# Performance work log

Measured on AMD Instinct MI355X. Metric: run time of the kernel, lower is better.

## Reference

```python
import jax, jax.numpy as jnp
import numpy as np

B, S, HID, NH, KCLIP = 2, 1500, 1024, 16, 64
HD = HID // NH  # 64


def setup_inputs() -> dict:
    key = jax.random.key(0)
    ks = jax.random.split(key, 16)
    std = 0.02
    inp = {
        "query": jax.random.normal(ks[0], (B, S, HID), jnp.float32),
        "key": jax.random.normal(ks[1], (B, S, HID), jnp.float32),
        "value": jax.random.normal(ks[2], (B, S, HID), jnp.float32),
        # per-head projection weights, stacked over heads: [NH, HID, HD]
        "Wq": jax.random.normal(ks[3], (NH, HID, HD), jnp.float32) * std,
        "bq": jax.random.normal(ks[4], (NH, HD), jnp.float32) * std,
        "Wk": jax.random.normal(ks[5], (NH, HID, HD), jnp.float32) * std,
        "bk": jax.random.normal(ks[6], (NH, HD), jnp.float32) * std,
        "Wv": jax.random.normal(ks[7], (NH, HID, HD), jnp.float32) * std,
        "bv": jax.random.normal(ks[8], (NH, HD), jnp.float32) * std,
        # Shaw relative-position embedding tables: [2k+1, HD]
        "pe_k": jax.random.normal(ks[9], (2 * KCLIP + 1, HD), jnp.float32) * std,
        "pe_v": jax.random.normal(ks[10], (2 * KCLIP + 1, HD), jnp.float32) * std,
        # output projection (torch Linear stored as x @ W + b here)
        "W_fc": jax.random.normal(ks[11], (HID, HID), jnp.float32) * std,
        "b_fc": jax.random.normal(ks[12], (HID,), jnp.float32) * std,
    }
    return inp


def _rel_bias(pe, length, k_clip):
    idx = jnp.arange(length)
    dist = jnp.clip(idx[None, :] - idx[:, None], -k_clip, k_clip) + k_clip
    return pe[dist]  # [S, S, HD]


def reference(query, key, value, Wq, bq, Wk, bk, Wv, bv, pe_k, pe_v, W_fc, b_fc):
    head_dim = Wq.shape[-1]
    seq = query.shape[1]
    k_clip = (pe_k.shape[0] - 1) // 2

    kb = _rel_bias(pe_k, seq, k_clip)  # [S, S, HD]
    vb = _rel_bias(pe_v, seq, k_clip)  # [S, S, HD]

    # batched per-head projections: [B, NH, S, HD]
    Q = jnp.einsum('bsh,nhd->bnsd', query, Wq) + bq[None, :, None, :]
    K = jnp.einsum('bsh,nhd->bnsd', key, Wk) + bk[None, :, None, :]
    V = jnp.einsum('bsh,nhd->bnsd', value, Wv) + bv[None, :, None, :]

    # content term + Shaw relative-key bias term
    scores = jnp.einsum('bnqd,bnkd->bnqk', Q, K) \
           + jnp.einsum('bnqd,qkd->bnqk', Q, kb)
    scores = scores / jnp.sqrt(jnp.asarray(head_dim, scores.dtype))

    w = jax.nn.softmax(scores, axis=-1)  # [B, NH, S, S]

    out = jnp.einsum('bnqk,bnkd->bnqd', w, V) \
        + jnp.einsum('bnqk,qkd->bnqd', w, vb)

    # concat heads (head order matches ModuleList concatenation)
    hidden = out.transpose(0, 2, 1, 3).reshape(query.shape[0], seq, -1)
    return hidden @ W_fc + b_fc
```

## Files before the change

### kernel.cpp

```cpp
#include <hip/hip_runtime.h>
#include <math.h>

#define B_     2
#define S_     1500
#define HID_   1024
#define NH_    16
#define HD_    64
#define M_     (B_*S_)
#define SP_    1536

typedef short bf16x8 __attribute__((ext_vector_type(8)));
typedef short bf16x4 __attribute__((ext_vector_type(4)));
typedef float f32x4  __attribute__((ext_vector_type(4)));

__device__ __forceinline__ float b2f(short s) {
    unsigned u = ((unsigned)(unsigned short)s) << 16;
    return __uint_as_float(u);
}
__device__ __forceinline__ short f2b(float f) {
    unsigned u = __float_as_uint(f);
    unsigned r = (u + 0x7FFFu + ((u >> 16) & 1u)) >> 16;
    return (short)r;
}
__device__ __forceinline__ void gload16(const short* src, short* lds) {
    __builtin_amdgcn_global_load_lds(
        (const __attribute__((address_space(1))) void*)src,
        (__attribute__((address_space(3))) void*)lds, 16, 0, 0);
}

__global__ __launch_bounds__(256) void cvt_act3(
    const float* __restrict__ q, const float* __restrict__ k,
    const float* __restrict__ v, short* __restrict__ oq,
    short* __restrict__ ok, short* __restrict__ ov)
{
    const float* src = blockIdx.y == 0 ? q : blockIdx.y == 1 ? k : v;
    short* dst       = blockIdx.y == 0 ? oq : blockIdx.y == 1 ? ok : ov;
    int i = blockIdx.x * 256 + threadIdx.x;
    const float4* p = (const float4*)(src + (size_t)i * 8);
    float4 a = p[0], b = p[1];
    bf16x8 o;
    o[0]=f2b(a.x); o[1]=f2b(a.y); o[2]=f2b(a.z); o[3]=f2b(a.w);
    o[4]=f2b(b.x); o[5]=f2b(b.y); o[6]=f2b(b.z); o[7]=f2b(b.w);
    *(bf16x8*)(dst + (size_t)i * 8) = o;
}

__global__ __launch_bounds__(256) void prep_w(
    const float* __restrict__ Wq, const float* __restrict__ Wk,
    const float* __restrict__ Wv, const float* __restrict__ Wfc,
    const float* __restrict__ pe_k, const float* __restrict__ pe_v,
    short* __restrict__ Wqt, short* __restrict__ Wkt, short* __restrict__ Wvt,
    short* __restrict__ Wfh, short* __restrict__ Wfl,
    short* __restrict__ pe_kb, short* __restrict__ pe_vt)
{
    int z = blockIdx.x, tid = threadIdx.x;
    if (z == 1024) {
        for (int s = tid; s < 144 * 64; s += 256) {
            int j = s >> 6, d = s & 63;
            pe_kb[s] = (j < 129) ? f2b(pe_k[j * 64 + d]) : (short)0;
        }
        for (int s = tid; s < 64 * 160; s += 256) {
            int d = s / 160, j = s - d * 160;
            pe_vt[s] = (j < 129) ? f2b(pe_v[j * 64 + d]) : (short)0;
        }
        return;
    }
    __shared__ float T[64][65];
    const float* src; short* dhi; short* dlo = nullptr;
    int C, c0, r0; float scale = 1.f;
    if (z < 768) {
        int widx = z >> 8, rem = z & 255;
        int h = rem >> 4, rt = rem & 15;
        src = (widx == 0 ? Wq : widx == 1 ? Wk : Wv) + (size_t)h * 1024 * 64;
        dhi = (widx == 0 ? Wqt : widx == 1 ? Wkt : Wvt) + (size_t)h * 64 * 1024;
        scale = (widx == 0) ? 0.125f : 1.0f;
        C = 64; c0 = 0; r0 = rt * 64;
    } else {
        int idx = z - 768;
        src = Wfc; dhi = Wfh; dlo = Wfl;
        C = 1024; c0 = (idx >> 4) * 64; r0 = (idx & 15) * 64;
    }
#pragma unroll
    for (int i = 0; i < 4; ++i) {
        int slot = tid + i * 256;
        int r = slot >> 4, cg = (slot & 15) * 4;
        float4 v = *(const float4*)(src + (size_t)(r0 + r) * C + c0 + cg);
        T[r][cg+0] = v.x*scale; T[r][cg+1] = v.y*scale;
        T[r][cg+2] = v.z*scale; T[r][cg+3] = v.w*scale;
    }
    __syncthreads();
#pragma unroll
    for (int i = 0; i < 16; ++i) {
        int slot = tid + i * 256;
        int c = slot >> 6, r = slot & 63;
        float v = T[r][c];
        short hi = f2b(v);
        size_t o = (size_t)(c0 + c) * 1024 + r0 + r;
        dhi[o] = hi;
        if (dlo) dlo[o] = f2b(v - b2f(hi));
    }
}

__device__ __forceinline__ void gemm_core(
    const short* __restrict__ Ahi, const short* __restrict__ Alo,
    const short* __restrict__ Bhi, const short* __restrict__ Blo,
    int kIters, int m0, int n0, short* As, short* Bs, f32x4 (&acc)[4][4])
{
    const int tid = threadIdx.x, w = tid >> 6, lane = tid & 63;
    const int l15 = lane & 15, lr4 = lane >> 4;
    const int wr = w >> 1, wc = w & 1;

    for (int it = 0; it < kIters; ++it) {
        int kt = it * 64;
        int seg = kt >> 10, kk0 = kt & 1023;
        const short* Aseg = (seg == 1) ? Alo : Ahi;
        const short* Bseg = (seg == 2) ? Blo : Bhi;
        __syncthreads();
#pragma unroll
        for (int c = 0; c < 4; ++c) {
            int slot = (w * 4 + c) * 64 + lane;
            int r = slot >> 3, cb = slot & 7;
            int sm = m0 + r; sm = sm < M_ ? sm : M_ - 1;
            gload16(Aseg + (size_t)sm * 1024 + kk0 + ((cb ^ (r & 7)) * 8),
                    As + (size_t)(w * 4 + c) * 512);
            gload16(Bseg + (size_t)(n0 + r) * 1024 + kk0 + ((cb ^ (r & 7)) * 8),
                    Bs + (size_t)(w * 4 + c) * 512);
        }
        __syncthreads();
#pragma unroll
        for (int kh = 0; kh < 2; ++kh) {
            bf16x8 aF[4], bF[4];
#pragma unroll
            for (int mi = 0; mi < 4; ++mi) {
                int r = wr * 64 + mi * 16 + l15;
                aF[mi] = *(const bf16x8*)(As + r * 64 + (((kh*4+lr4) ^ (r & 7)) * 8));
            }
#pragma unroll
            for (int ni = 0; ni < 4; ++ni) {
                int r = wc * 64 + ni * 16 + l15;
                bF[ni] = *(const bf16x8*)(Bs + r * 64 + (((kh*4+lr4) ^ (r & 7)) * 8));
            }
#pragma unroll
            for (int mi = 0; mi < 4; ++mi)
#pragma unroll
                for (int ni = 0; ni < 4; ++ni)
                    acc[mi][ni] = __builtin_amdgcn_mfma_f32_16x16x32_bf16(
                        aF[mi], bF[ni], acc[mi][ni], 0, 0, 0);
        }
    }
}

__global__ __launch_bounds__(256) void gemm_qkv(
    const short* __restrict__ qb, const short* __restrict__ kb,
    const short* __restrict__ vb, const short* __restrict__ Wqt,
    const short* __restrict__ Wkt, const short* __restrict__ Wvt,
    const float* __restrict__ bq, const float* __restrict__ bk,
    const float* __restrict__ bv,
    short* __restrict__ Qp, short* __restrict__ Kp, short* __restrict__ Vp)
{
    __shared__ short As[128 * 64];
    __shared__ short Bs[128 * 64];
    const int z = blockIdx.z;
    const short* A  = z == 0 ? qb : z == 1 ? kb : vb;
    const short* Bw = z == 0 ? Wqt : z == 1 ? Wkt : Wvt;
    const float* bias = z == 0 ? bq : z == 1 ? bk : bv;
    const float bscale = z == 0 ? 0.125f : 1.0f;
    short* out = z == 0 ? Qp : z == 1 ? Kp : Vp;
    const int m0 = blockIdx.x * 128, n0 = blockIdx.y * 128;

    f32x4 zf = {0.f,0.f,0.f,0.f};
    f32x4 acc[4][4];
#pragma unroll
    for (int i = 0; i < 4; ++i)
#pragma unroll
        for (int j = 0; j < 4; ++j) acc[i][j] = zf;

    gemm_core(A, A, Bw, Bw, 16, m0, n0, As, Bs, acc);

    const int tid = threadIdx.x, w = tid >> 6, lane = tid & 63;
    const int l15 = lane & 15, lr4 = lane >> 4;
    const int wr = w >> 1, wc = w & 1;
#pragma unroll
    for (int mi = 0; mi < 4; ++mi)
#pragma unroll
        for (int rr = 0; rr < 4; ++rr) {
            int m = m0 + wr * 64 + mi * 16 + lr4 * 4 + rr;
            if (m >= M_) continue;
            int b = m / S_, s = m - b * S_;
#pragma unroll
            for (int ni = 0; ni < 4; ++ni) {
                int n = n0 + wc * 64 + ni * 16 + l15;
                float v = acc[mi][ni][rr] + bias[n] * bscale;
                int h = n >> 6, d = n & 63;
                out[(((size_t)(b * NH_ + h)) * S_ + s) * HD_ + d] = f2b(v);
            }
        }
}

__global__ __launch_bounds__(256) void gemm_fc(
    const short* __restrict__ Ahi, const short* __restrict__ Alo,
    const short* __restrict__ Bhi, const short* __restrict__ Blo,
    const float* __restrict__ bias, float* __restrict__ out)
{
    __shared__ short As[128 * 64];
    __shared__ short Bs[128 * 64];
    const int m0 = blockIdx.x * 128, n0 = blockIdx.y * 128;
    f32x4 zf = {0.f,0.f,0.f,0.f};
    f32x4 acc[4][4];
#pragma unroll
    for (int i = 0; i < 4; ++i)
#pragma unroll
        for (int j = 0; j < 4; ++j) acc[i][j] = zf;

    gemm_core(Ahi, Alo, Bhi, Blo, 48, m0, n0, As, Bs, acc);

    const int tid = threadIdx.x, w = tid >> 6, lane = tid & 63;
    const int l15 = lane & 15, lr4 = lane >> 4;
    const int wr = w >> 1, wc = w & 1;
#pragma unroll
    for (int mi = 0; mi < 4; ++mi)
#pragma unroll
        for (int rr = 0; rr < 4; ++rr) {
            int m = m0 + wr * 64 + mi * 16 + lr4 * 4 + rr;
            if (m >= M_) continue;
#pragma unroll
            for (int ni = 0; ni < 4; ++ni) {
                int n = n0 + wc * 64 + ni * 16 + l15;
                out[(size_t)m * 1024 + n] = acc[mi][ni][rr] + bias[n];
            }
        }
}

__global__ __launch_bounds__(256) void vtrans(
    const short* __restrict__ Vp, short* __restrict__ Vtg)
{
    __shared__ short T[64][72];
    const int bh = blockIdx.y, s0 = blockIdx.x * 64, tid = threadIdx.x;
    const size_t kv = (size_t)bh * S_ * 64;
#pragma unroll
    for (int i = 0; i < 2; ++i) {
        int slot = tid + i * 256;
        int r = slot >> 3, cb = slot & 7;
        int ss = s0 + r; ss = ss < S_ ? ss : S_ - 1;
        bf16x8 v = *(const bf16x8*)(Vp + kv + (size_t)ss * 64 + cb * 8);
        *(bf16x8*)(&T[r][cb * 8]) = v;
    }
    __syncthreads();
#pragma unroll
    for (int i = 0; i < 2; ++i) {
        int slot = tid + i * 256;
        int d = slot >> 3, cg = slot & 7;
        bf16x8 v;
#pragma unroll
        for (int j = 0; j < 8; ++j) v[j] = T[cg * 8 + j][d];
        *(bf16x8*)(Vtg + ((size_t)bh * 64 + d) * SP_ + s0 + cg * 8) = v;
    }
}

__global__ __launch_bounds__(256) void attn_mfma(
    const short* __restrict__ Qb, const short* __restrict__ Kb,
    const short* __restrict__ Vtg, const short* __restrict__ pe_kb,
    const short* __restrict__ pe_vt,
    short* __restrict__ hid_hi, short* __restrict__ hid_lo)
{
    __shared__ short Kc[64 * 64];
    __shared__ short Vt[64 * 64];
    __shared__ short qpe[64 * 144];
    __shared__ short wsm[64 * 160];
    __shared__ short Pw[4][16 * 64];

    const int tid = threadIdx.x, w = tid >> 6, lane = tid & 63;
    const int l15 = lane & 15, lr4 = lane >> 4;
    const int bh = blockIdx.y, q0 = blockIdx.x * 64;
    const int qw = q0 + w * 16;
    const int myq = qw + l15;
    const int myrow = w * 16 + l15;
    const size_t kv  = (size_t)bh * S_ * HD_;
    const size_t vtb = (size_t)bh * 64 * SP_;
    const int swz = (l15 & 7) << 1;

    {
        short ini = f2b(-1e30f);
        bf16x8 iv;
#pragma unroll
        for (int i = 0; i < 8; ++i) iv[i] = ini;
        for (int s = tid; s < 64 * 160 / 8; s += 256)
            *(bf16x8*)(wsm + (size_t)s * 8) = iv;
    }
#pragma unroll
    for (int c = 0; c < 2; ++c) {
        int slot = (w * 2 + c) * 64 + lane;
        int r = slot >> 3, cb = slot & 7;
        int sq = q0 + r; sq = sq < S_ ? sq : S_ - 1;
        gload16(Qb + kv + (size_t)sq * 64 + ((cb ^ (r & 7)) * 8),
                Kc + (size_t)(w * 2 + c) * 512);
    }
    __syncthreads();

    bf16x8 qA[2];
    {
        int r = myrow;
        qA[0] = *(const bf16x8*)(Kc + r * 64 + ((lr4 ^ (r & 7)) * 8));
        qA[1] = *(const bf16x8*)(Kc + r * 64 + (((4 + lr4) ^ (r & 7)) * 8));
    }

    f32x4 zf = {0.f,0.f,0.f,0.f};
#pragma unroll
    for (int jt = 0; jt < 9; ++jt) {
        f32x4 a = zf;
#pragma unroll
        for (int kh = 0; kh < 2; ++kh) {
            bf16x8 pf = *(const bf16x8*)(pe_kb + (size_t)(jt * 16 + l15) * 64 + kh * 32 + lr4 * 8);
            a = __builtin_amdgcn_mfma_f32_16x16x32_bf16(pf, qA[kh], a, 0, 0, 0);
        }
        bf16x4 pk;
#pragma unroll
        for (int rr = 0; rr < 4; ++rr) pk[rr] = f2b(a[rr]);
        *(bf16x4*)(qpe + (size_t)myrow * 144 + jt * 16 + lr4 * 4) = pk;
    }
    __syncthreads();

    const float qpe0   = b2f(qpe[myrow * 144 + 0]);
    const float qpe128 = b2f(qpe[myrow * 144 + 128]);

    float m = -1e30f, s0s = 0.f, s1s = 0.f;
    f32x4 o[4];
#pragma unroll
    for (int t = 0; t < 4; ++t) o[t] = zf;

    for (int c = 0; c < 24; ++c) {
        const int kc = c * 64;
        __syncthreads();
#pragma unroll
        for (int cc = 0; cc < 2; ++cc) {
            int slot = (w * 2 + cc) * 64 + lane;
            int r = slot >> 3, cb = slot & 7;
            int sk = kc + r; sk = sk < S_ ? sk : S_ - 1;
            gload16(Kb + kv + (size_t)sk * 64 + ((cb ^ (r & 7)) * 8),
                    Kc + (size_t)(w * 2 + cc) * 512);
            gload16(Vtg + vtb + (size_t)r * SP_ + kc + ((cb ^ (r & 7)) * 8),
                    Vt + (size_t)(w * 2 + cc) * 512);
        }
        __syncthreads();

        f32x4 sa[4];
#pragma unroll
        for (int t = 0; t < 4; ++t) {
            sa[t] = zf;
#pragma unroll
            for (int kh = 0; kh < 2; ++kh) {
                int r = t * 16 + l15;
                bf16x8 kB = *(const bf16x8*)(Kc + r * 64 + (((kh*4+lr4) ^ (r & 7)) * 8));
                sa[t] = __builtin_amdgcn_mfma_f32_16x16x32_bf16(kB, qA[kh], sa[t], 0, 0, 0);
            }
        }

        const bool all_lo = (kc + 63 - qw) <= -64;
        const bool all_hi = (kc - (qw + 15)) >= 64;
        const bool mixed  = !(all_lo || all_hi);
        const float ubias = all_lo ? qpe0 : qpe128;

        float lg[4][4];
        float rm = -1e30f;
#pragma unroll
        for (int t = 0; t < 4; ++t)
#pragma unroll
            for (int rr = 0; rr < 4; ++rr) {
                int k = kc + t * 16 + lr4 * 4 + rr;
                int rel = k - myq;
                float v;
                if (mixed) {
                    int jc = rel < -64 ? 0 : (rel > 64 ? 128 : rel + 64);
                    v = sa[t][rr] + b2f(qpe[myrow * 144 + jc]);
                } else {
                    v = sa[t][rr] + ubias;
                }
                if (k >= S_) v = -1e30f;
                lg[t][rr] = v;
                rm = fmaxf(rm, v);
                if (mixed && rel > -64 && rel < 64)
                    wsm[myrow * 160 + rel + 64] = f2b(v);
            }
        rm = fmaxf(rm, __shfl_xor(rm, 16));
        rm = fmaxf(rm, __shfl_xor(rm, 32));

        if (__any(rm > m)) {
            float nm = fmaxf(m, rm);
            float fac = __expf(m - nm);
            m = nm; s0s *= fac; s1s *= fac;
            float fo[4];
#pragma unroll
            for (int rr = 0; rr < 4; ++rr) fo[rr] = __shfl(fac, lr4 * 4 + rr);
#pragma unroll
            for (int t = 0; t < 4; ++t)
#pragma unroll
                for (int rr = 0; rr < 4; ++rr) o[t][rr] *= fo[rr];
        }

        float ls0 = 0.f, ls1 = 0.f;
#pragma unroll
        for (int t = 0; t < 4; ++t) {
            bf16x4 pk;
#pragma unroll
            for (int rr = 0; rr < 4; ++rr) {
                float p = __expf(lg[t][rr] - m);
                pk[rr] = f2b(p);
                if (mixed) {
                    int rel = (kc + t * 16 + lr4 * 4 + rr) - myq;
                    if (rel <= -64) ls0 += p; else if (rel >= 64) ls1 += p;
                } else if (all_lo) ls0 += p; else ls1 += p;
            }
            *(bf16x4*)(Pw[w] + l15 * 64 + (((t * 4 + lr4) ^ swz) << 2)) = pk;
        }
        ls0 += __shfl_xor(ls0, 16); ls0 += __shfl_xor(ls0, 32);
        ls1 += __shfl_xor(ls1, 16); ls1 += __shfl_xor(ls1, 32);
        s0s += ls0; s1s += ls1;

#pragma unroll
        for (int win = 0; win < 2; ++win) {
            bf16x8 pA = *(const bf16x8*)(Pw[w] + l15 * 64 + (((win * 8 + lr4 * 2) ^ swz) << 2));
#pragma unroll
            for (int td = 0; td < 4; ++td) {
                int r = td * 16 + l15;
                bf16x8 vB = *(const bf16x8*)(Vt + r * 64 + (((win*4+lr4) ^ (r & 7)) * 8));
                o[td] = __builtin_amdgcn_mfma_f32_16x16x32_bf16(pA, vB, o[td], 0, 0, 0);
            }
        }
    }

    short* rowp = wsm + (size_t)myrow * 160;
    float midsum = 0.f;
#pragma unroll
    for (int cc = 0; cc < 5; ++cc) {
        int off = (cc * 4 + lr4) * 8;
        bf16x8 mv = *(const bf16x8*)(rowp + off);
        bf16x8 ev;
#pragma unroll
        for (int jj = 0; jj < 8; ++jj) {
            float e = __expf(b2f(mv[jj]) - m);
            ev[jj] = f2b(e);
            midsum += e;
        }
        *(bf16x8*)(rowp + off) = ev;
    }
    midsum += __shfl_xor(midsum, 16); midsum += __shfl_xor(midsum, 32);
    const float linv = 1.f / (s0s + s1s + midsum);
    if (lr4 == 0) { rowp[0] = f2b(s0s); rowp[128] = f2b(s1s); }

#pragma unroll
    for (int jh = 0; jh < 5; ++jh) {
        bf16x8 aW = *(const bf16x8*)(wsm + (size_t)myrow * 160 + jh * 32 + lr4 * 8);
#pragma unroll
        for (int td = 0; td < 4; ++td) {
            bf16x8 bW = *(const bf16x8*)(pe_vt + (size_t)(td * 16 + l15) * 160 + jh * 32 + lr4 * 8);
            o[td] = __builtin_amdgcn_mfma_f32_16x16x32_bf16(aW, bW, o[td], 0, 0, 0);
        }
    }

    {
        float fo[4];
#pragma unroll
        for (int rr = 0; rr < 4; ++rr) fo[rr] = __shfl(linv, lr4 * 4 + rr);
#pragma unroll
        for (int td = 0; td < 4; ++td)
#pragma unroll
            for (int rr = 0; rr < 4; ++rr) o[td][rr] *= fo[rr];
    }

#pragma unroll
    for (int td = 0; td < 4; ++td)
#pragma unroll
        for (int rr = 0; rr < 4; ++rr) {
            int qrow = lr4 * 4 + rr;
            int d = td * 16 + l15;
            int inner = (((d >> 2) ^ ((qrow & 7) << 1)) << 2) + (d & 3);
            float v = o[td][rr];
            short hi = f2b(v);
            Pw[w][qrow * 64 + inner] = hi;
            wsm[(w * 16 + qrow) * 160 + inner] = f2b(v - b2f(hi));
        }
    {
        int b = bh >> 4, h = bh & 15;
        int qrow = lane >> 2;
        int q = q0 + w * 16 + qrow;
#pragma unroll
        for (int i = 0; i < 2; ++i) {
            int cb = (lane & 3) * 2 + i;
            int qws = (cb * 2) ^ ((qrow & 7) << 1);
            bf16x8 hv = *(const bf16x8*)(Pw[w] + qrow * 64 + qws * 4);
            bf16x8 lv = *(const bf16x8*)(wsm + (w * 16 + qrow) * 160 + qws * 4);
            if (q < S_) {
                size_t oo = ((size_t)(b * S_ + q)) * 1024 + h * 64 + cb * 8;
                *(bf16x8*)(hid_hi + oo) = hv;
                *(bf16x8*)(hid_lo + oo) = lv;
            }
        }
    }
}

extern "C" void kernel_launch(void* const* d_in, const int* in_sizes, int n_in,
                              void* d_out, int out_size, void* d_ws, size_t ws_size,
                              hipStream_t stream)
{
    const float* query = (const float*)d_in[0];
    const float* key   = (const float*)d_in[1];
    const float* value = (const float*)d_in[2];
    const float* Wq    = (const float*)d_in[3];
    const float* bq    = (const float*)d_in[4];
    const float* Wk    = (const float*)d_in[5];
    const float* bk    = (const float*)d_in[6];
    const float* Wv    = (const float*)d_in[7];
    const float* bv    = (const float*)d_in[8];
    const float* pe_k  = (const float*)d_in[9];
    const float* pe_v  = (const float*)d_in[10];
    const float* W_fc  = (const float*)d_in[11];
    const float* b_fc  = (const float*)d_in[12];

    char* W = (char*)d_ws;
    short* qb   = (short*)(W + 0);
    short* kb   = (short*)(W + 6291456);
    short* vb   = (short*)(W + 12582912);
    short* Vtg  = vb;
    short* Wqt  = (short*)(W + 18874368);
    short* Wkt  = (short*)(W + 20971520);
    short* Wvt  = (short*)(W + 23068672);
    short* Wfh  = (short*)(W + 25165824);
    short* Wfl  = (short*)(W + 27262976);
    short* Qp   = (short*)(W + 29360128);
    short* Kp   = (short*)(W + 35651584);
    short* Vp   = (short*)(W + 41943040);
    short* pekb = (short*)(W + 48234496);
    short* pevt = (short*)(W + 48252928);
    short* hidh = qb;
    short* hidl = kb;

    cvt_act3<<<dim3(1500, 3), 256, 0, stream>>>(query, key, value, qb, kb, vb);
    prep_w<<<1025, 256, 0, stream>>>(Wq, Wk, Wv, W_fc, pe_k, pe_v,
                                     Wqt, Wkt, Wvt, Wfh, Wfl, pekb, pevt);
    gemm_qkv<<<dim3(24, 8, 3), 256, 0, stream>>>(qb, kb, vb, Wqt, Wkt, Wvt,
                                                 bq, bk, bv, Qp, Kp, Vp);
    vtrans<<<dim3(24, 32), 256, 0, stream>>>(Vp, Vtg);
    attn_mfma<<<dim3(24, 32), 256, 0, stream>>>(Qp, Kp, Vtg, pekb, pevt, hidh, hidl);
    gemm_fc<<<dim3(24, 8), 256, 0, stream>>>(hidh, hidl, Wfh, Wfl, b_fc, (float*)d_out);
}
```

Baseline: 284.3 us.

## Double-buffer K/V tiles in attention, use exp2 softmax with lazy rescale

The attention kernel now double-buffers the K and V LDS tiles, prefetching the next chunk with async global-to-LDS loads while the current one is computed, and relies on explicit waitcnt plus barriers instead of two __syncthreads per iteration. Q is prescaled by log2(e) so the softmax uses exp2f, and the running-max rescale is skipped unless the max grows by more than 8 (in log2 units). The grid is remapped to a 1D launch with a block swizzle intended to group heads across XCDs, and s_setprio is raised around the MFMA sections. The extra LDS buffers lower occupancy, and the deferred rescale lets intermediate exponentials grow larger, which carries some bf16 precision risk.

```diff
diff --git a/kernel.cpp b/kernel.cpp
--- a/kernel.cpp
+++ b/kernel.cpp
@@ -8,6 +8,7 @@
 #define HD_    64
 #define M_     (B_*S_)
 #define SP_    1536
+#define LOG2E  1.4426950408889634f
 
 typedef short bf16x8 __attribute__((ext_vector_type(8)));
 typedef short bf16x4 __attribute__((ext_vector_type(4)));
@@ -26,6 +27,11 @@
     __builtin_amdgcn_global_load_lds(
         (const __attribute__((address_space(1))) void*)src,
         (__attribute__((address_space(3))) void*)lds, 16, 0, 0);
+}
+__device__ __forceinline__ void bar() {
+    asm volatile("" ::: "memory");
+    __builtin_amdgcn_s_barrier();
+    asm volatile("" ::: "memory");
 }
 
 __global__ __launch_bounds__(256) void cvt_act3(
@@ -72,7 +78,7 @@
         int h = rem >> 4, rt = rem & 15;
         src = (widx == 0 ? Wq : widx == 1 ? Wk : Wv) + (size_t)h * 1024 * 64;
         dhi = (widx == 0 ? Wqt : widx == 1 ? Wkt : Wvt) + (size_t)h * 64 * 1024;
-        scale = (widx == 0) ? 0.125f : 1.0f;
+        scale = (widx == 0) ? 0.125f * LOG2E : 1.0f;
         C = 64; c0 = 0; r0 = rt * 64;
     } else {
         int idx = z - 768;
@@ -163,7 +169,7 @@
     const short* A  = z == 0 ? qb : z == 1 ? kb : vb;
     const short* Bw = z == 0 ? Wqt : z == 1 ? Wkt : Wvt;
     const float* bias = z == 0 ? bq : z == 1 ? bk : bv;
-    const float bscale = z == 0 ? 0.125f : 1.0f;
+    const float bscale = z == 0 ? 0.125f * LOG2E : 1.0f;
     short* out = z == 0 ? Qp : z == 1 ? Kp : Vp;
     const int m0 = blockIdx.x * 128, n0 = blockIdx.y * 128;
 
@@ -262,15 +268,17 @@
     const short* __restrict__ pe_vt,
     short* __restrict__ hid_hi, short* __restrict__ hid_lo)
 {
-    __shared__ short Kc[64 * 64];
-    __shared__ short Vt[64 * 64];
+    __shared__ short Kc[2][4096];
+    __shared__ short Vt[2][4096];
     __shared__ short qpe[64 * 144];
     __shared__ short wsm[64 * 160];
     __shared__ short Pw[4][16 * 64];
 
     const int tid = threadIdx.x, w = tid >> 6, lane = tid & 63;
     const int l15 = lane & 15, lr4 = lane >> 4;
-    const int bh = blockIdx.y, q0 = blockIdx.x * 64;
+    const int lg = (blockIdx.x & 7) * 96 + (blockIdx.x >> 3);
+    const int bh = lg / 24, bx = lg - bh * 24;
+    const int q0 = bx * 64;
     const int qw = q0 + w * 16;
     const int myq = qw + l15;
     const int myrow = w * 16 + l15;
@@ -283,24 +291,37 @@
         bf16x8 iv;
 #pragma unroll
         for (int i = 0; i < 8; ++i) iv[i] = ini;
-        for (int s = tid; s < 64 * 160 / 8; s += 256)
-            *(bf16x8*)(wsm + (size_t)s * 8) = iv;
-    }
-#pragma unroll
-    for (int c = 0; c < 2; ++c) {
-        int slot = (w * 2 + c) * 64 + lane;
+        short* base = wsm + w * 16 * 160;
+#pragma unroll
+        for (int i = 0; i < 5; ++i)
+            *(bf16x8*)(base + (size_t)(i * 64 + lane) * 8) = iv;
+    }
+#pragma unroll
+    for (int cc = 0; cc < 2; ++cc) {
+        int slot = (w * 2 + cc) * 64 + lane;
         int r = slot >> 3, cb = slot & 7;
         int sq = q0 + r; sq = sq < S_ ? sq : S_ - 1;
         gload16(Qb + kv + (size_t)sq * 64 + ((cb ^ (r & 7)) * 8),
-                Kc + (size_t)(w * 2 + c) * 512);
-    }
-    __syncthreads();
+                &Kc[1][(w * 2 + cc) * 512]);
+    }
+#pragma unroll
+    for (int cc = 0; cc < 2; ++cc) {
+        int slot = (w * 2 + cc) * 64 + lane;
+        int r = slot >> 3, cb = slot & 7;
+        gload16(Kb + kv + (size_t)r * 64 + ((cb ^ (r & 7)) * 8),
+                &Kc[0][(w * 2 + cc) * 512]);
+        gload16(Vtg + vtb + (size_t)r * SP_ + ((cb ^ (r & 7)) * 8),
+                &Vt[0][(w * 2 + cc) * 512]);
+    }
+    asm volatile("s_waitcnt vmcnt(4)" ::: "memory");
+    __builtin_amdgcn_s_barrier();
+    asm volatile("" ::: "memory");
 
     bf16x8 qA[2];
     {
         int r = myrow;
-        qA[0] = *(const bf16x8*)(Kc + r * 64 + ((lr4 ^ (r & 7)) * 8));
-        qA[1] = *(const bf16x8*)(Kc + r * 64 + (((4 + lr4) ^ (r & 7)) * 8));
+        qA[0] = *(const bf16x8*)(&Kc[1][r * 64 + ((lr4 ^ (r & 7)) * 8)]);
+        qA[1] = *(const bf16x8*)(&Kc[1][r * 64 + (((4 + lr4) ^ (r & 7)) * 8)]);
     }
 
     f32x4 zf = {0.f,0.f,0.f,0.f};
@@ -317,10 +338,9 @@
         for (int rr = 0; rr < 4; ++rr) pk[rr] = f2b(a[rr]);
         *(bf16x4*)(qpe + (size_t)myrow * 144 + jt * 16 + lr4 * 4) = pk;
     }
-    __syncthreads();
-
     const float qpe0   = b2f(qpe[myrow * 144 + 0]);
     const float qpe128 = b2f(qpe[myrow * 144 + 128]);
+    bar();
 
     float m = -1e30f, s0s = 0.f, s1s = 0.f;
     f32x4 o[4];
@@ -329,19 +349,30 @@
 
     for (int c = 0; c < 24; ++c) {
         const int kc = c * 64;
-        __syncthreads();
-#pragma unroll
-        for (int cc = 0; cc < 2; ++cc) {
-            int slot = (w * 2 + cc) * 64 + lane;
-            int r = slot >> 3, cb = slot & 7;
-            int sk = kc + r; sk = sk < S_ ? sk : S_ - 1;
-            gload16(Kb + kv + (size_t)sk * 64 + ((cb ^ (r & 7)) * 8),
-                    Kc + (size_t)(w * 2 + cc) * 512);
-            gload16(Vtg + vtb + (size_t)r * SP_ + kc + ((cb ^ (r & 7)) * 8),
-                    Vt + (size_t)(w * 2 + cc) * 512);
-        }
-        __syncthreads();
-
+        const int p = c & 1;
+        if (c < 23) {
+            const int kcn = kc + 64;
+            short* KD = Kc[1 - p]; short* VD = Vt[1 - p];
+#pragma unroll
+            for (int cc = 0; cc < 2; ++cc) {
+                int slot = (w * 2 + cc) * 64 + lane;
+                int r = slot >> 3, cb = slot & 7;
+                int sk = kcn + r; sk = sk < S_ ? sk : S_ - 1;
+                gload16(Kb + kv + (size_t)sk * 64 + ((cb ^ (r & 7)) * 8),
+                        KD + (w * 2 + cc) * 512);
+                gload16(Vtg + vtb + (size_t)r * SP_ + kcn + ((cb ^ (r & 7)) * 8),
+                        VD + (w * 2 + cc) * 512);
+            }
+            asm volatile("s_waitcnt vmcnt(4)" ::: "memory");
+        } else {
+            asm volatile("s_waitcnt vmcnt(0)" ::: "memory");
+        }
+        __builtin_amdgcn_s_barrier();
+        asm volatile("" ::: "memory");
+
+        const short* KP = Kc[p]; const short* VP = Vt[p];
+
+        __builtin_amdgcn_s_setprio(1);
         f32x4 sa[4];
 #pragma unroll
         for (int t = 0; t < 4; ++t) {
@@ -349,17 +380,18 @@
 #pragma unroll
             for (int kh = 0; kh < 2; ++kh) {
                 int r = t * 16 + l15;
-                bf16x8 kB = *(const bf16x8*)(Kc + r * 64 + (((kh*4+lr4) ^ (r & 7)) * 8));
+                bf16x8 kB = *(const bf16x8*)(KP + r * 64 + (((kh*4+lr4) ^ (r & 7)) * 8));
                 sa[t] = __builtin_amdgcn_mfma_f32_16x16x32_bf16(kB, qA[kh], sa[t], 0, 0, 0);
             }
         }
+        __builtin_amdgcn_s_setprio(0);
 
         const bool all_lo = (kc + 63 - qw) <= -64;
         const bool all_hi = (kc - (qw + 15)) >= 64;
         const bool mixed  = !(all_lo || all_hi);
         const float ubias = all_lo ? qpe0 : qpe128;
 
-        float lg[4][4];
+        float lg2[4][4];
         float rm = -1e30f;
 #pragma unroll
         for (int t = 0; t < 4; ++t)
@@ -375,7 +407,7 @@
                     v = sa[t][rr] + ubias;
                 }
                 if (k >= S_) v = -1e30f;
-                lg[t][rr] = v;
+                lg2[t][rr] = v;
                 rm = fmaxf(rm, v);
                 if (mixed && rel > -64 && rel < 64)
                     wsm[myrow * 160 + rel + 64] = f2b(v);
@@ -383,9 +415,9 @@
         rm = fmaxf(rm, __shfl_xor(rm, 16));
         rm = fmaxf(rm, __shfl_xor(rm, 32));
 
-        if (__any(rm > m)) {
+        if (!__all(rm <= m + 8.f)) {
             float nm = fmaxf(m, rm);
-            float fac = __expf(m - nm);
+            float fac = exp2f(m - nm);
             m = nm; s0s *= fac; s1s *= fac;
             float fo[4];
 #pragma unroll
@@ -402,12 +434,12 @@
             bf16x4 pk;
 #pragma unroll
             for (int rr = 0; rr < 4; ++rr) {
-                float p = __expf(lg[t][rr] - m);
-                pk[rr] = f2b(p);
+                float p2 = exp2f(lg2[t][rr] - m);
+                pk[rr] = f2b(p2);
                 if (mixed) {
                     int rel = (kc + t * 16 + lr4 * 4 + rr) - myq;
-                    if (rel <= -64) ls0 += p; else if (rel >= 64) ls1 += p;
-                } else if (all_lo) ls0 += p; else ls1 += p;
+                    if (rel <= -64) ls0 += p2; else if (rel >= 64) ls1 += p2;
+                } else if (all_lo) ls0 += p2; else ls1 += p2;
             }
             *(bf16x4*)(Pw[w] + l15 * 64 + (((t * 4 + lr4) ^ swz) << 2)) = pk;
         }
@@ -415,16 +447,20 @@
         ls1 += __shfl_xor(ls1, 16); ls1 += __shfl_xor(ls1, 32);
         s0s += ls0; s1s += ls1;
 
+        __builtin_amdgcn_s_setprio(1);
 #pragma unroll
         for (int win = 0; win < 2; ++win) {
             bf16x8 pA = *(const bf16x8*)(Pw[w] + l15 * 64 + (((win * 8 + lr4 * 2) ^ swz) << 2));
 #pragma unroll
             for (int td = 0; td < 4; ++td) {
                 int r = td * 16 + l15;
-                bf16x8 vB = *(const bf16x8*)(Vt + r * 64 + (((win*4+lr4) ^ (r & 7)) * 8));
+                bf16x8 vB = *(const bf16x8*)(VP + r * 64 + (((win*4+lr4) ^ (r & 7)) * 8));
                 o[td] = __builtin_amdgcn_mfma_f32_16x16x32_bf16(pA, vB, o[td], 0, 0, 0);
             }
         }
+        __builtin_amdgcn_s_setprio(0);
+
+        bar();
     }
 
     short* rowp = wsm + (size_t)myrow * 160;
@@ -436,7 +472,7 @@
         bf16x8 ev;
 #pragma unroll
         for (int jj = 0; jj < 8; ++jj) {
-            float e = __expf(b2f(mv[jj]) - m);
+            float e = exp2f(b2f(mv[jj]) - m);
             ev[jj] = f2b(e);
             midsum += e;
         }
@@ -539,6 +575,6 @@
     gemm_qkv<<<dim3(24, 8, 3), 256, 0, stream>>>(qb, kb, vb, Wqt, Wkt, Wvt,
                                                  bq, bk, bv, Qp, Kp, Vp);
     vtrans<<<dim3(24, 32), 256, 0, stream>>>(Vp, Vtg);
-    attn_mfma<<<dim3(24, 32), 256, 0, stream>>>(Qp, Kp, Vtg, pekb, pevt, hidh, hidl);
+    attn_mfma<<<768, 256, 0, stream>>>(Qp, Kp, Vtg, pekb, pevt, hidh, hidl);
     gemm_fc<<<dim3(24, 8), 256, 0, stream>>>(hidh, hidl, Wfh, Wfl, b_fc, (float*)d_out);
 }
```

Result: no change. 284.3 us (-0.0%).
